# Kernel optimization log

Measured on AMD Instinct MI355X. Metric: run time of the kernel, lower is better.

## Reference

```python
import jax, jax.numpy as jnp
import numpy as np
from jax import lax

C = 256
B, H, W = 8, 64, 64


def dwconv(x, w, b, pad):
    # x: [B,C,H,W], w: [C,1,kh,kw] depthwise (groups=C), b: [C]
    y = lax.conv_general_dilated(
        x, w,
        window_strides=(1, 1),
        padding=pad,
        dimension_numbers=('NCHW', 'OIHW', 'NCHW'),
        feature_group_count=x.shape[1],
    )
    return y + b[None, :, None, None]


def setup_inputs() -> dict:
    key = jax.random.key(0)
    ks = jax.random.split(key, 16)
    s = 0.05
    inp = {
        'x': jax.random.normal(ks[0], (B, C, H, W), jnp.float32),
        'w0':   jax.random.normal(ks[1], (C, 1, 5, 5), jnp.float32) * s,
        'b0':   jax.random.normal(ks[2], (C,), jnp.float32) * s,
        'w0_1': jax.random.normal(ks[3], (C, 1, 1, 7), jnp.float32) * s,
        'b0_1': jax.random.normal(ks[4], (C,), jnp.float32) * s,
        'w0_2': jax.random.normal(ks[5], (C, 1, 7, 1), jnp.float32) * s,
        'b0_2': jax.random.normal(ks[6], (C,), jnp.float32) * s,
        'w1_1': jax.random.normal(ks[7], (C, 1, 1, 11), jnp.float32) * s,
        'b1_1': jax.random.normal(ks[8], (C,), jnp.float32) * s,
        'w1_2': jax.random.normal(ks[9], (C, 1, 11, 1), jnp.float32) * s,
        'b1_2': jax.random.normal(ks[10], (C,), jnp.float32) * s,
        'w2_1': jax.random.normal(ks[11], (C, 1, 1, 21), jnp.float32) * s,
        'b2_1': jax.random.normal(ks[12], (C,), jnp.float32) * s,
        'w2_2': jax.random.normal(ks[13], (C, 1, 21, 1), jnp.float32) * s,
        'b2_2': jax.random.normal(ks[14], (C,), jnp.float32) * s,
    }
    return inp


def reference(x, w0, b0, w0_1, b0_1, w0_2, b0_2,
              w1_1, b1_1, w1_2, b1_2, w2_1, b2_1, w2_2, b2_2):
    # 5x5 depthwise, pad 2
    attn = dwconv(x, w0, b0, ((2, 2), (2, 2)))
    # stage 0: 1x7 / 7x1 strips
    a0x = dwconv(attn, w0_1, b0_1, ((0, 0), (3, 3)))
    a0y = dwconv(attn, w0_2, b0_2, ((3, 3), (0, 0)))
    attn_0 = a0x * a0y
    # stage 1: 1x11 / 11x1 strips
    a1x = dwconv(a0x, w1_1, b1_1, ((0, 0), (5, 5)))
    a1y = dwconv(a0y, w1_2, b1_2, ((5, 5), (0, 0)))
    attn_1 = a1x * a1y
    # stage 2: 1x21 / 21x1 strips
    a2x = dwconv(a1x, w2_1, b2_1, ((0, 0), (10, 10)))
    a2y = dwconv(a1y, w2_2, b2_2, ((10, 10), (0, 0)))
    attn_2 = a2x * a2y
    return (attn_0, attn_1, attn_2)
```

## Files before the change

kernel.cpp:

```cpp
#include <hip/hip_runtime.h>


#define YS 68
#define R1_SZ 4624
#define LDS_WORDS (R1_SZ + 4352)

__device__ __forceinline__ float dpp_prev(float v) {
    return __int_as_float(__builtin_amdgcn_update_dpp(
        0, __float_as_int(v), 0x111, 0xF, 0xF, false));
}
__device__ __forceinline__ float dpp_next(float v) {
    return __int_as_float(__builtin_amdgcn_update_dpp(
        0, __float_as_int(v), 0x101, 0xF, 0xF, false));
}
__device__ __forceinline__ void ld4(const float* p, float* f) {
    float4 q = *(const float4*)p;
    f[0] = q.x; f[1] = q.y; f[2] = q.z; f[3] = q.w;
}
__device__ __forceinline__ void st4(float* p, float a, float b, float c, float d) {
    float4 q; q.x = a; q.y = b; q.z = c; q.w = d;
    *(float4*)p = q;
}

__global__ __launch_bounds__(256, 4)
void msca_fused(const float* __restrict__ x,
                const float* __restrict__ w0,   const float* __restrict__ b0,
                const float* __restrict__ w0_1, const float* __restrict__ b0_1,
                const float* __restrict__ w0_2, const float* __restrict__ b0_2,
                const float* __restrict__ w1_1, const float* __restrict__ b1_1,
                const float* __restrict__ w1_2, const float* __restrict__ b1_2,
                const float* __restrict__ w2_1, const float* __restrict__ b2_1,
                const float* __restrict__ w2_2, const float* __restrict__ b2_2,
                float* __restrict__ out)
{
    __shared__ __align__(16) float lds[LDS_WORDS];
    float* R1 = lds;
    float* R2 = lds + R1_SZ;

    const int t     = threadIdx.x;
    const int plane = blockIdx.x;
    const int ch    = plane & 255;
    const int r  = t >> 2;
    const int jg = t & 3;
    const int j0 = jg << 4;
    const int c  = t & 63;
    const int i0 = (t >> 6) << 4;

    const float* xg = x + (size_t)plane * 4096;
    float* o0 = out + (size_t)plane * 4096;
    float* o1 = o0 + 8388608;
    float* o2 = o1 + 8388608;

    float xR[16];
    #pragma unroll
    for (int k = 0; k < 4; k++) ld4(&xg[r * 64 + j0 + 4 * k], &xR[4 * k]);

    #pragma unroll
    for (int k0 = 0; k0 < 2; k0++) {
        int k = t + 256 * k0;
        if (k < 272) R1[k < 136 ? k : k + 4352] = 0.f;
    }
    if (t < 64) {
        int b = (t + 2) * YS;
        R1[b] = 0.f; R1[b + 1] = 0.f; R1[b + 66] = 0.f; R1[b + 67] = 0.f;
    }
    {
        float* row = &R1[(r + 2) * YS];
        float2 e0; e0.x = xR[0];  e0.y = xR[1];  *(float2*)&row[j0 + 2]  = e0;
        st4(&row[j0 + 4],  xR[2],  xR[3],  xR[4],  xR[5]);
        st4(&row[j0 + 8],  xR[6],  xR[7],  xR[8],  xR[9]);
        st4(&row[j0 + 12], xR[10], xR[11], xR[12], xR[13]);
        float2 e1; e1.x = xR[14]; e1.y = xR[15]; *(float2*)&row[j0 + 16] = e1;
    }
    __syncthreads();

    float attnR[16];
    {
        const float bb = b0[ch];
        #pragma unroll
        for (int j = 0; j < 16; j++) attnR[j] = bb;
        #pragma unroll
        for (int dr = 0; dr < 5; dr++) {
            float f[20];
            if (dr == 2) {
                float e0 = dpp_prev(xR[14]), e1 = dpp_prev(xR[15]);
                float e2 = dpp_next(xR[0]),  e3 = dpp_next(xR[1]);
                f[0] = jg ? e0 : 0.f;  f[1] = jg ? e1 : 0.f;
                #pragma unroll
                for (int k = 0; k < 16; k++) f[2 + k] = xR[k];
                f[18] = (jg < 3) ? e2 : 0.f;  f[19] = (jg < 3) ? e3 : 0.f;
            } else {
                const float* row = &R1[(r + dr) * YS + j0];
                #pragma unroll
                for (int k = 0; k < 5; k++) ld4(&row[4 * k], &f[4 * k]);
            }
            #pragma unroll
            for (int v = 0; v < 5; v++) {
                const float ww = w0[ch * 25 + dr * 5 + v];
                #pragma unroll
                for (int j = 0; j < 16; j++) attnR[j] += ww * f[j + v];
            }
        }
        float* row = &R2[r * YS];
        st4(&row[j0],      attnR[0],  attnR[1],  attnR[2],  attnR[3]);
        st4(&row[j0 + 4],  attnR[4],  attnR[5],  attnR[6],  attnR[7]);
        st4(&row[j0 + 8],  attnR[8],  attnR[9],  attnR[10], attnR[11]);
        st4(&row[j0 + 12], attnR[12], attnR[13], attnR[14], attnR[15]);
    }
    __syncthreads();

    float a0xR[16];
    {
        const float bb = b0_1[ch];
        float av[22];
        float p13 = dpp_prev(attnR[13]), p14 = dpp_prev(attnR[14]), p15 = dpp_prev(attnR[15]);
        float n0  = dpp_next(attnR[0]),  n1  = dpp_next(attnR[1]),  n2  = dpp_next(attnR[2]);
        av[0] = jg ? p13 : 0.f;  av[1] = jg ? p14 : 0.f;  av[2] = jg ? p15 : 0.f;
        #pragma unroll
        for (int k = 0; k < 16; k++) av[3 + k] = attnR[k];
        av[19] = (jg < 3) ? n0 : 0.f;  av[20] = (jg < 3) ? n1 : 0.f;  av[21] = (jg < 3) ? n2 : 0.f;
        #pragma unroll
        for (int j = 0; j < 16; j++) a0xR[j] = bb;
        #pragma unroll
        for (int v = 0; v < 7; v++) {
            const float ww = w0_1[ch * 7 + v];
            #pragma unroll
            for (int j = 0; j < 16; j++) a0xR[j] += ww * av[j + v];
        }
    }
    float a0yR[16];
    {
        const float bb = b0_2[ch];
        float cv[22];
        #pragma unroll
        for (int d = 0; d < 22; d++) {
            const int ir = i0 + d - 3;
            cv[d] = ((unsigned)ir <= 63u) ? R2[ir * YS + c] : 0.f;
        }
        #pragma unroll
        for (int ii = 0; ii < 16; ii++) a0yR[ii] = bb;
        #pragma unroll
        for (int u = 0; u < 7; u++) {
            const float ww = w0_2[ch * 7 + u];
            #pragma unroll
            for (int ii = 0; ii < 16; ii++) a0yR[ii] += ww * cv[ii + u];
        }
        #pragma unroll
        for (int ii = 0; ii < 16; ii++) R1[(i0 + ii) * YS + c] = a0yR[ii];
    }
    __syncthreads();

    #pragma unroll
    for (int k = 0; k < 4; k++) {
        float f[4]; ld4(&R1[r * YS + j0 + 4 * k], f);
        st4(&o0[r * 64 + j0 + 4 * k],
            a0xR[4 * k] * f[0], a0xR[4 * k + 1] * f[1],
            a0xR[4 * k + 2] * f[2], a0xR[4 * k + 3] * f[3]);
    }
    float a1xR[16];
    {
        const float bb = b1_1[ch];
        float xv[26];
        #pragma unroll
        for (int d = 0; d < 5; d++) {
            float p = dpp_prev(a0xR[11 + d]);
            float n = dpp_next(a0xR[d]);
            xv[d]      = jg ? p : 0.f;
            xv[21 + d] = (jg < 3) ? n : 0.f;
        }
        #pragma unroll
        for (int k = 0; k < 16; k++) xv[5 + k] = a0xR[k];
        #pragma unroll
        for (int j = 0; j < 16; j++) a1xR[j] = bb;
        #pragma unroll
        for (int v = 0; v < 11; v++) {
            const float ww = w1_1[ch * 11 + v];
            #pragma unroll
            for (int j = 0; j < 16; j++) a1xR[j] += ww * xv[j + v];
        }
    }
    float a1yR[16];
    {
        const float bb = b1_2[ch];
        float yv[26];
        #pragma unroll
        for (int d = 0; d < 5; d++)  yv[d]      = i0        ? R1[(i0 - 5 + d) * YS + c]  : 0.f;
        #pragma unroll
        for (int k = 0; k < 16; k++) yv[5 + k]  = a0yR[k];
        #pragma unroll
        for (int d = 0; d < 5; d++)  yv[21 + d] = (i0 < 48) ? R1[(i0 + 16 + d) * YS + c] : 0.f;
        #pragma unroll
        for (int ii = 0; ii < 16; ii++) a1yR[ii] = bb;
        #pragma unroll
        for (int u = 0; u < 11; u++) {
            const float ww = w1_2[ch * 11 + u];
            #pragma unroll
            for (int ii = 0; ii < 16; ii++) a1yR[ii] += ww * yv[ii + u];
        }
        #pragma unroll
        for (int ii = 0; ii < 16; ii++) R2[(i0 + ii) * YS + c] = a1yR[ii];
    }
    __syncthreads();

    #pragma unroll
    for (int k = 0; k < 4; k++) {
        float f[4]; ld4(&R2[r * YS + j0 + 4 * k], f);
        st4(&o1[r * 64 + j0 + 4 * k],
            a1xR[4 * k] * f[0], a1xR[4 * k + 1] * f[1],
            a1xR[4 * k + 2] * f[2], a1xR[4 * k + 3] * f[3]);
    }
    float a2xR[16];
    {
        const float bb = b2_1[ch];
        float xv[36];
        #pragma unroll
        for (int d = 0; d < 10; d++) {
            float p = dpp_prev(a1xR[6 + d]);
            float n = dpp_next(a1xR[d]);
            xv[d]      = jg ? p : 0.f;
            xv[26 + d] = (jg < 3) ? n : 0.f;
        }
        #pragma unroll
        for (int k = 0; k < 16; k++) xv[10 + k] = a1xR[k];
        #pragma unroll
        for (int j = 0; j < 16; j++) a2xR[j] = bb;
        #pragma unroll
        for (int v = 0; v < 21; v++) {
            const float ww = w2_1[ch * 21 + v];
            #pragma unroll
            for (int j = 0; j < 16; j++) a2xR[j] += ww * xv[j + v];
        }
    }
    {
        const float bb = b2_2[ch];
        float yv[36];
        #pragma unroll
        for (int d = 0; d < 10; d++) yv[d]      = i0        ? R2[(i0 - 10 + d) * YS + c] : 0.f;
        #pragma unroll
        for (int k = 0; k < 16; k++) yv[10 + k] = a1yR[k];
        #pragma unroll
        for (int d = 0; d < 10; d++) yv[26 + d] = (i0 < 48) ? R2[(i0 + 16 + d) * YS + c] : 0.f;
        float a2yR[16];
        #pragma unroll
        for (int ii = 0; ii < 16; ii++) a2yR[ii] = bb;
        #pragma unroll
        for (int u = 0; u < 21; u++) {
            const float ww = w2_2[ch * 21 + u];
            #pragma unroll
            for (int ii = 0; ii < 16; ii++) a2yR[ii] += ww * yv[ii + u];
        }
        #pragma unroll
        for (int ii = 0; ii < 16; ii++) R1[(i0 + ii) * YS + c] = a2yR[ii];
    }
    __syncthreads();

    #pragma unroll
    for (int k = 0; k < 4; k++) {
        float f[4]; ld4(&R1[r * YS + j0 + 4 * k], f);
        st4(&o2[r * 64 + j0 + 4 * k],
            a2xR[4 * k] * f[0], a2xR[4 * k + 1] * f[1],
            a2xR[4 * k + 2] * f[2], a2xR[4 * k + 3] * f[3]);
    }
}

extern "C" void kernel_launch(void* const* d_in, const int* in_sizes, int n_in,
                              void* d_out, int out_size, void* d_ws, size_t ws_size,
                              hipStream_t stream) {
    msca_fused<<<2048, 256, 0, stream>>>(
        (const float*)d_in[0],
        (const float*)d_in[1],  (const float*)d_in[2],
        (const float*)d_in[3],  (const float*)d_in[4],
        (const float*)d_in[5],  (const float*)d_in[6],
        (const float*)d_in[7],  (const float*)d_in[8],
        (const float*)d_in[9],  (const float*)d_in[10],
        (const float*)d_in[11], (const float*)d_in[12],
        (const float*)d_in[13], (const float*)d_in[14],
        (float*)d_out);
}
```

Measured before the change: 46.05 us.

## Process two channel planes per block to amortize barriers and add ILP

Each block now handles two (batch, channel) planes instead of one, with each stage looping over both planes between barriers. This halves the grid, roughly doubles LDS per block, and lowers launch bounds to 2 blocks per CU. The aim is to share each __syncthreads across two planes and give the scheduler independent work to interleave. In exchange, register pressure rises sharply (several 2x16 arrays live at once), which risks spills and lower occupancy.

```diff
diff --git a/kernel.cpp b/kernel.cpp
--- a/kernel.cpp
+++ b/kernel.cpp
@@ -2,8 +2,9 @@
 
 
 #define YS 68
-#define R1_SZ 4624
-#define LDS_WORDS (R1_SZ + 4352)
+#define R1W 4624
+#define R2W 4352
+#define LDS_WORDS (2 * (R1W + R2W))
 
 __device__ __forceinline__ float dpp_prev(float v) {
     return __int_as_float(__builtin_amdgcn_update_dpp(
@@ -22,7 +23,7 @@
     *(float4*)p = q;
 }
 
-__global__ __launch_bounds__(256, 4)
+__global__ __launch_bounds__(256, 2)
 void msca_fused(const float* __restrict__ x,
                 const float* __restrict__ w0,   const float* __restrict__ b0,
                 const float* __restrict__ w0_1, const float* __restrict__ b0_1,
@@ -34,63 +35,66 @@
                 float* __restrict__ out)
 {
     __shared__ __align__(16) float lds[LDS_WORDS];
-    float* R1 = lds;
-    float* R2 = lds + R1_SZ;
-
-    const int t     = threadIdx.x;
-    const int plane = blockIdx.x;
-    const int ch    = plane & 255;
+
+    const int t  = threadIdx.x;
     const int r  = t >> 2;
     const int jg = t & 3;
     const int j0 = jg << 4;
     const int c  = t & 63;
     const int i0 = (t >> 6) << 4;
 
-    const float* xg = x + (size_t)plane * 4096;
-    float* o0 = out + (size_t)plane * 4096;
-    float* o1 = o0 + 8388608;
-    float* o2 = o1 + 8388608;
-
-    float xR[16];
-    #pragma unroll
-    for (int k = 0; k < 4; k++) ld4(&xg[r * 64 + j0 + 4 * k], &xR[4 * k]);
-
-    #pragma unroll
-    for (int k0 = 0; k0 < 2; k0++) {
-        int k = t + 256 * k0;
-        if (k < 272) R1[k < 136 ? k : k + 4352] = 0.f;
-    }
-    if (t < 64) {
-        int b = (t + 2) * YS;
-        R1[b] = 0.f; R1[b + 1] = 0.f; R1[b + 66] = 0.f; R1[b + 67] = 0.f;
-    }
-    {
-        float* row = &R1[(r + 2) * YS];
-        float2 e0; e0.x = xR[0];  e0.y = xR[1];  *(float2*)&row[j0 + 2]  = e0;
-        st4(&row[j0 + 4],  xR[2],  xR[3],  xR[4],  xR[5]);
-        st4(&row[j0 + 8],  xR[6],  xR[7],  xR[8],  xR[9]);
-        st4(&row[j0 + 12], xR[10], xR[11], xR[12], xR[13]);
-        float2 e1; e1.x = xR[14]; e1.y = xR[15]; *(float2*)&row[j0 + 16] = e1;
-    }
-    __syncthreads();
-
-    float attnR[16];
-    {
+    const int plane0 = blockIdx.x * 2;
+
+    float xR[2][16], attnR[2][16], a0xR[2][16], a0yR[2][16];
+    float a1xR[2][16], a1yR[2][16], a2xR[2][16];
+
+    #pragma unroll
+    for (int p = 0; p < 2; p++) {
+        const float* xg = x + (size_t)(plane0 + p) * 4096;
+        #pragma unroll
+        for (int k = 0; k < 4; k++) ld4(&xg[r * 64 + j0 + 4 * k], &xR[p][4 * k]);
+    }
+    #pragma unroll
+    for (int p = 0; p < 2; p++) {
+        float* R1p = lds + p * R1W;
+        #pragma unroll
+        for (int k0 = 0; k0 < 2; k0++) {
+            int k = t + 256 * k0;
+            if (k < 272) R1p[k < 136 ? k : k + 4352] = 0.f;
+        }
+        if (t < 64) {
+            int b = (t + 2) * YS;
+            R1p[b] = 0.f; R1p[b + 1] = 0.f; R1p[b + 66] = 0.f; R1p[b + 67] = 0.f;
+        }
+        float* row = &R1p[(r + 2) * YS];
+        float2 e0; e0.x = xR[p][0];  e0.y = xR[p][1];  *(float2*)&row[j0 + 2]  = e0;
+        st4(&row[j0 + 4],  xR[p][2],  xR[p][3],  xR[p][4],  xR[p][5]);
+        st4(&row[j0 + 8],  xR[p][6],  xR[p][7],  xR[p][8],  xR[p][9]);
+        st4(&row[j0 + 12], xR[p][10], xR[p][11], xR[p][12], xR[p][13]);
+        float2 e1; e1.x = xR[p][14]; e1.y = xR[p][15]; *(float2*)&row[j0 + 16] = e1;
+    }
+    __syncthreads();
+
+    #pragma unroll
+    for (int p = 0; p < 2; p++) {
+        const int ch = (plane0 + p) & 255;
+        float* R1p = lds + p * R1W;
+        float* R2p = lds + 2 * R1W + p * R2W;
         const float bb = b0[ch];
         #pragma unroll
-        for (int j = 0; j < 16; j++) attnR[j] = bb;
+        for (int j = 0; j < 16; j++) attnR[p][j] = bb;
         #pragma unroll
         for (int dr = 0; dr < 5; dr++) {
             float f[20];
             if (dr == 2) {
-                float e0 = dpp_prev(xR[14]), e1 = dpp_prev(xR[15]);
-                float e2 = dpp_next(xR[0]),  e3 = dpp_next(xR[1]);
+                float e0 = dpp_prev(xR[p][14]), e1 = dpp_prev(xR[p][15]);
+                float e2 = dpp_next(xR[p][0]),  e3 = dpp_next(xR[p][1]);
                 f[0] = jg ? e0 : 0.f;  f[1] = jg ? e1 : 0.f;
                 #pragma unroll
-                for (int k = 0; k < 16; k++) f[2 + k] = xR[k];
+                for (int k = 0; k < 16; k++) f[2 + k] = xR[p][k];
                 f[18] = (jg < 3) ? e2 : 0.f;  f[19] = (jg < 3) ? e3 : 0.f;
             } else {
-                const float* row = &R1[(r + dr) * YS + j0];
+                const float* row = &R1p[(r + dr) * YS + j0];
                 #pragma unroll
                 for (int k = 0; k < 5; k++) ld4(&row[4 * k], &f[4 * k]);
             }
@@ -98,175 +102,203 @@
             for (int v = 0; v < 5; v++) {
                 const float ww = w0[ch * 25 + dr * 5 + v];
                 #pragma unroll
-                for (int j = 0; j < 16; j++) attnR[j] += ww * f[j + v];
+                for (int j = 0; j < 16; j++) attnR[p][j] += ww * f[j + v];
             }
         }
-        float* row = &R2[r * YS];
-        st4(&row[j0],      attnR[0],  attnR[1],  attnR[2],  attnR[3]);
-        st4(&row[j0 + 4],  attnR[4],  attnR[5],  attnR[6],  attnR[7]);
-        st4(&row[j0 + 8],  attnR[8],  attnR[9],  attnR[10], attnR[11]);
-        st4(&row[j0 + 12], attnR[12], attnR[13], attnR[14], attnR[15]);
-    }
-    __syncthreads();
-
-    float a0xR[16];
-    {
+        float* row = &R2p[r * YS];
+        st4(&row[j0],      attnR[p][0],  attnR[p][1],  attnR[p][2],  attnR[p][3]);
+        st4(&row[j0 + 4],  attnR[p][4],  attnR[p][5],  attnR[p][6],  attnR[p][7]);
+        st4(&row[j0 + 8],  attnR[p][8],  attnR[p][9],  attnR[p][10], attnR[p][11]);
+        st4(&row[j0 + 12], attnR[p][12], attnR[p][13], attnR[p][14], attnR[p][15]);
+    }
+    __syncthreads();
+
+    #pragma unroll
+    for (int p = 0; p < 2; p++) {
+        const int ch = (plane0 + p) & 255;
         const float bb = b0_1[ch];
         float av[22];
-        float p13 = dpp_prev(attnR[13]), p14 = dpp_prev(attnR[14]), p15 = dpp_prev(attnR[15]);
-        float n0  = dpp_next(attnR[0]),  n1  = dpp_next(attnR[1]),  n2  = dpp_next(attnR[2]);
+        float p13 = dpp_prev(attnR[p][13]), p14 = dpp_prev(attnR[p][14]), p15 = dpp_prev(attnR[p][15]);
+        float n0  = dpp_next(attnR[p][0]),  n1  = dpp_next(attnR[p][1]),  n2  = dpp_next(attnR[p][2]);
         av[0] = jg ? p13 : 0.f;  av[1] = jg ? p14 : 0.f;  av[2] = jg ? p15 : 0.f;
         #pragma unroll
-        for (int k = 0; k < 16; k++) av[3 + k] = attnR[k];
+        for (int k = 0; k < 16; k++) av[3 + k] = attnR[p][k];
         av[19] = (jg < 3) ? n0 : 0.f;  av[20] = (jg < 3) ? n1 : 0.f;  av[21] = (jg < 3) ? n2 : 0.f;
         #pragma unroll
-        for (int j = 0; j < 16; j++) a0xR[j] = bb;
+        for (int j = 0; j < 16; j++) a0xR[p][j] = bb;
         #pragma unroll
         for (int v = 0; v < 7; v++) {
             const float ww = w0_1[ch * 7 + v];
             #pragma unroll
-            for (int j = 0; j < 16; j++) a0xR[j] += ww * av[j + v];
-        }
-    }
-    float a0yR[16];
-    {
+            for (int j = 0; j < 16; j++) a0xR[p][j] += ww * av[j + v];
+        }
+    }
+    #pragma unroll
+    for (int p = 0; p < 2; p++) {
+        const int ch = (plane0 + p) & 255;
+        float* R1p = lds + p * R1W;
+        float* R2p = lds + 2 * R1W + p * R2W;
         const float bb = b0_2[ch];
         float cv[22];
         #pragma unroll
         for (int d = 0; d < 22; d++) {
             const int ir = i0 + d - 3;
-            cv[d] = ((unsigned)ir <= 63u) ? R2[ir * YS + c] : 0.f;
-        }
-        #pragma unroll
-        for (int ii = 0; ii < 16; ii++) a0yR[ii] = bb;
+            cv[d] = ((unsigned)ir <= 63u) ? R2p[ir * YS + c] : 0.f;
+        }
+        #pragma unroll
+        for (int ii = 0; ii < 16; ii++) a0yR[p][ii] = bb;
         #pragma unroll
         for (int u = 0; u < 7; u++) {
             const float ww = w0_2[ch * 7 + u];
             #pragma unroll
-            for (int ii = 0; ii < 16; ii++) a0yR[ii] += ww * cv[ii + u];
-        }
-        #pragma unroll
-        for (int ii = 0; ii < 16; ii++) R1[(i0 + ii) * YS + c] = a0yR[ii];
-    }
-    __syncthreads();
-
-    #pragma unroll
-    for (int k = 0; k < 4; k++) {
-        float f[4]; ld4(&R1[r * YS + j0 + 4 * k], f);
-        st4(&o0[r * 64 + j0 + 4 * k],
-            a0xR[4 * k] * f[0], a0xR[4 * k + 1] * f[1],
-            a0xR[4 * k + 2] * f[2], a0xR[4 * k + 3] * f[3]);
-    }
-    float a1xR[16];
-    {
+            for (int ii = 0; ii < 16; ii++) a0yR[p][ii] += ww * cv[ii + u];
+        }
+        #pragma unroll
+        for (int ii = 0; ii < 16; ii++) R1p[(i0 + ii) * YS + c] = a0yR[p][ii];
+    }
+    __syncthreads();
+
+    #pragma unroll
+    for (int p = 0; p < 2; p++) {
+        float* R1p = lds + p * R1W;
+        float* o0 = out + (size_t)(plane0 + p) * 4096;
+        #pragma unroll
+        for (int k = 0; k < 4; k++) {
+            float f[4]; ld4(&R1p[r * YS + j0 + 4 * k], f);
+            st4(&o0[r * 64 + j0 + 4 * k],
+                a0xR[p][4 * k] * f[0], a0xR[p][4 * k + 1] * f[1],
+                a0xR[p][4 * k + 2] * f[2], a0xR[p][4 * k + 3] * f[3]);
+        }
+    }
+    #pragma unroll
+    for (int p = 0; p < 2; p++) {
+        const int ch = (plane0 + p) & 255;
         const float bb = b1_1[ch];
         float xv[26];
         #pragma unroll
         for (int d = 0; d < 5; d++) {
-            float p = dpp_prev(a0xR[11 + d]);
-            float n = dpp_next(a0xR[d]);
-            xv[d]      = jg ? p : 0.f;
-            xv[21 + d] = (jg < 3) ? n : 0.f;
-        }
-        #pragma unroll
-        for (int k = 0; k < 16; k++) xv[5 + k] = a0xR[k];
-        #pragma unroll
-        for (int j = 0; j < 16; j++) a1xR[j] = bb;
+            float pp = dpp_prev(a0xR[p][11 + d]);
+            float nn = dpp_next(a0xR[p][d]);
+            xv[d]      = jg ? pp : 0.f;
+            xv[21 + d] = (jg < 3) ? nn : 0.f;
+        }
+        #pragma unroll
+        for (int k = 0; k < 16; k++) xv[5 + k] = a0xR[p][k];
+        #pragma unroll
+        for (int j = 0; j < 16; j++) a1xR[p][j] = bb;
         #pragma unroll
         for (int v = 0; v < 11; v++) {
             const float ww = w1_1[ch * 11 + v];
             #pragma unroll
-            for (int j = 0; j < 16; j++) a1xR[j] += ww * xv[j + v];
-        }
-    }
-    float a1yR[16];
-    {
+            for (int j = 0; j < 16; j++) a1xR[p][j] += ww * xv[j + v];
+        }
+    }
+    #pragma unroll
+    for (int p = 0; p < 2; p++) {
+        const int ch = (plane0 + p) & 255;
+        float* R1p = lds + p * R1W;
+        float* R2p = lds + 2 * R1W + p * R2W;
         const float bb = b1_2[ch];
         float yv[26];
         #pragma unroll
-        for (int d = 0; d < 5; d++)  yv[d]      = i0        ? R1[(i0 - 5 + d) * YS + c]  : 0.f;
-        #pragma unroll
-        for (int k = 0; k < 16; k++) yv[5 + k]  = a0yR[k];
-        #pragma unroll
-        for (int d = 0; d < 5; d++)  yv[21 + d] = (i0 < 48) ? R1[(i0 + 16 + d) * YS + c] : 0.f;
-        #pragma unroll
-        for (int ii = 0; ii < 16; ii++) a1yR[ii] = bb;
+        for (int d = 0; d < 5; d++)  yv[d]      = i0        ? R1p[(i0 - 5 + d) * YS + c]  : 0.f;
+        #pragma unroll
+        for (int k = 0; k < 16; k++) yv[5 + k]  = a0yR[p][k];
+        #pragma unroll
+        for (int d = 0; d < 5; d++)  yv[21 + d] = (i0 < 48) ? R1p[(i0 + 16 + d) * YS + c] : 0.f;
+        #pragma unroll
+        for (int ii = 0; ii < 16; ii++) a1yR[p][ii] = bb;
         #pragma unroll
         for (int u = 0; u < 11; u++) {
             const float ww = w1_2[ch * 11 + u];
             #pragma unroll
-            for (int ii = 0; ii < 16; ii++) a1yR[ii] += ww * yv[ii + u];
-        }
-        #pragma unroll
-        for (int ii = 0; ii < 16; ii++) R2[(i0 + ii) * YS + c] = a1yR[ii];
-    }
-    __syncthreads();
-
-    #pragma unroll
-    for (int k = 0; k < 4; k++) {
-        float f[4]; ld4(&R2[r * YS + j0 + 4 * k], f);
-        st4(&o1[r * 64 + j0 + 4 * k],
-            a1xR[4 * k] * f[0], a1xR[4 * k + 1] * f[1],
-            a1xR[4 * k + 2] * f[2], a1xR[4 * k + 3] * f[3]);
-    }
-    float a2xR[16];
-    {
+            for (int ii = 0; ii < 16; ii++) a1yR[p][ii] += ww * yv[ii + u];
+        }
+        #pragma unroll
+        for (int ii = 0; ii < 16; ii++) R2p[(i0 + ii) * YS + c] = a1yR[p][ii];
+    }
+    __syncthreads();
+
+    #pragma unroll
+    for (int p = 0; p < 2; p++) {
+        float* R2p = lds + 2 * R1W + p * R2W;
+        float* o1 = out + 8388608 + (size_t)(plane0 + p) * 4096;
+        #pragma unroll
+        for (int k = 0; k < 4; k++) {
+            float f[4]; ld4(&R2p[r * YS + j0 + 4 * k], f);
+            st4(&o1[r * 64 + j0 + 4 * k],
+                a1xR[p][4 * k] * f[0], a1xR[p][4 * k + 1] * f[1],
+                a1xR[p][4 * k + 2] * f[2], a1xR[p][4 * k + 3] * f[3]);
+        }
+    }
+    #pragma unroll
+    for (int p = 0; p < 2; p++) {
+        const int ch = (plane0 + p) & 255;
         const float bb = b2_1[ch];
         float xv[36];
         #pragma unroll
         for (int d = 0; d < 10; d++) {
-            float p = dpp_prev(a1xR[6 + d]);
-            float n = dpp_next(a1xR[d]);
-            xv[d]      = jg ? p : 0.f;
-            xv[26 + d] = (jg < 3) ? n : 0.f;
-        }
-        #pragma unroll
-        for (int k = 0; k < 16; k++) xv[10 + k] = a1xR[k];
-        #pragma unroll
-        for (int j = 0; j < 16; j++) a2xR[j] = bb;
+            float pp = dpp_prev(a1xR[p][6 + d]);
+            float nn = dpp_next(a1xR[p][d]);
+            xv[d]      = jg ? pp : 0.f;
+            xv[26 + d] = (jg < 3) ? nn : 0.f;
+        }
+        #pragma unroll
+        for (int k = 0; k < 16; k++) xv[10 + k] = a1xR[p][k];
+        #pragma unroll
+        for (int j = 0; j < 16; j++) a2xR[p][j] = bb;
         #pragma unroll
         for (int v = 0; v < 21; v++) {
             const float ww = w2_1[ch * 21 + v];
             #pragma unroll
-            for (int j = 0; j < 16; j++) a2xR[j] += ww * xv[j + v];
-        }
-    }
-    {
+            for (int j = 0; j < 16; j++) a2xR[p][j] += ww * xv[j + v];
+        }
+    }
+    #pragma unroll
+    for (int p = 0; p < 2; p++) {
+        const int ch = (plane0 + p) & 255;
+        float* R1p = lds + p * R1W;
+        float* R2p = lds + 2 * R1W + p * R2W;
         const float bb = b2_2[ch];
         float yv[36];
         #pragma unroll
-        for (int d = 0; d < 10; d++) yv[d]      = i0        ? R2[(i0 - 10 + d) * YS + c] : 0.f;
-        #pragma unroll
-        for (int k = 0; k < 16; k++) yv[10 + k] = a1yR[k];
-        #pragma unroll
-        for (int d = 0; d < 10; d++) yv[26 + d] = (i0 < 48) ? R2[(i0 + 16 + d) * YS + c] : 0.f;
-        float a2yR[16];
-        #pragma unroll
-        for (int ii = 0; ii < 16; ii++) a2yR[ii] = bb;
+        for (int d = 0; d < 10; d++) yv[d]      = i0        ? R2p[(i0 - 10 + d) * YS + c] : 0.f;
+        #pragma unroll
+        for (int k = 0; k < 16; k++) yv[10 + k] = a1yR[p][k];
+        #pragma unroll
+        for (int d = 0; d < 10; d++) yv[26 + d] = (i0 < 48) ? R2p[(i0 + 16 + d) * YS + c] : 0.f;
+        float a2y[16];
+        #pragma unroll
+        for (int ii = 0; ii < 16; ii++) a2y[ii] = bb;
         #pragma unroll
         for (int u = 0; u < 21; u++) {
             const float ww = w2_2[ch * 21 + u];
             #pragma unroll
-            for (int ii = 0; ii < 16; ii++) a2yR[ii] += ww * yv[ii + u];
-        }
-        #pragma unroll
-        for (int ii = 0; ii < 16; ii++) R1[(i0 + ii) * YS + c] = a2yR[ii];
-    }
-    __syncthreads();
-
-    #pragma unroll
-    for (int k = 0; k < 4; k++) {
-        float f[4]; ld4(&R1[r * YS + j0 + 4 * k], f);
-        st4(&o2[r * 64 + j0 + 4 * k],
-            a2xR[4 * k] * f[0], a2xR[4 * k + 1] * f[1],
-            a2xR[4 * k + 2] * f[2], a2xR[4 * k + 3] * f[3]);
+            for (int ii = 0; ii < 16; ii++) a2y[ii] += ww * yv[ii + u];
+        }
+        #pragma unroll
+        for (int ii = 0; ii < 16; ii++) R1p[(i0 + ii) * YS + c] = a2y[ii];
+    }
+    __syncthreads();
+
+    #pragma unroll
+    for (int p = 0; p < 2; p++) {
+        float* R1p = lds + p * R1W;
+        float* o2 = out + 2 * 8388608 + (size_t)(plane0 + p) * 4096;
+        #pragma unroll
+        for (int k = 0; k < 4; k++) {
+            float f[4]; ld4(&R1p[r * YS + j0 + 4 * k], f);
+            st4(&o2[r * 64 + j0 + 4 * k],
+                a2xR[p][4 * k] * f[0], a2xR[p][4 * k + 1] * f[1],
+                a2xR[p][4 * k + 2] * f[2], a2xR[p][4 * k + 3] * f[3]);
+        }
     }
 }
 
 extern "C" void kernel_launch(void* const* d_in, const int* in_sizes, int n_in,
                               void* d_out, int out_size, void* d_ws, size_t ws_size,
                               hipStream_t stream) {
-    msca_fused<<<2048, 256, 0, stream>>>(
+    msca_fused<<<1024, 256, 0, stream>>>(
         (const float*)d_in[0],
         (const float*)d_in[1],  (const float*)d_in[2],
         (const float*)d_in[3],  (const float*)d_in[4],
```

New measurement: 55.10 us. 19.6% more time.

## Vectorize depthwise conv accumulations with packed float2 FMAs and defer output stores

Applied to the files above, without the earlier changes.

Rewrites every stencil accumulation to operate on float2 pairs through a templated helper, so even-offset taps can map to packed FMA (v_pk_fma_f32) while odd taps stay scalar. Window arrays are rearranged into pair layout with padding slots. The stage-0 and stage-1 output products are computed early and their global stores are delayed until after later syncs, overlapping them with subsequent compute. This aims to cut VALU instruction count but raises register pressure under the 4-waves launch bound.

```diff
diff --git a/kernel.cpp b/kernel.cpp
--- a/kernel.cpp
+++ b/kernel.cpp
@@ -2,8 +2,11 @@
 
 
 #define YS 68
-#define R1_SZ 4624
-#define LDS_WORDS (R1_SZ + 4352)
+#define R1W 4624
+#define R2W 4352
+#define LDS_WORDS (R1W + R2W)
+
+typedef float v2f __attribute__((ext_vector_type(2)));
 
 __device__ __forceinline__ float dpp_prev(float v) {
     return __int_as_float(__builtin_amdgcn_update_dpp(
@@ -13,13 +16,34 @@
     return __int_as_float(__builtin_amdgcn_update_dpp(
         0, __float_as_int(v), 0x101, 0xF, 0xF, false));
 }
-__device__ __forceinline__ void ld4(const float* p, float* f) {
+__device__ __forceinline__ void ld4p(const float* p, v2f* w) {
     float4 q = *(const float4*)p;
-    f[0] = q.x; f[1] = q.y; f[2] = q.z; f[3] = q.w;
-}
-__device__ __forceinline__ void st4(float* p, float a, float b, float c, float d) {
-    float4 q; q.x = a; q.y = b; q.z = c; q.w = d;
+    w[0].x = q.x; w[0].y = q.y; w[1].x = q.z; w[1].y = q.w;
+}
+__device__ __forceinline__ void st4p(float* p, v2f a, v2f b) {
+    float4 q; q.x = a.x; q.y = a.y; q.z = b.x; q.w = b.y;
     *(float4*)p = q;
+}
+
+template<int K, int TAPOFF>
+__device__ __forceinline__ void conv_acc(const float* __restrict__ wrow,
+                                         const v2f* wnd, v2f* A) {
+    #pragma unroll
+    for (int v = 0; v < K; v++) {
+        const float w = wrow[v];
+        const int u = v + TAPOFF;
+        if ((u & 1) == 0) {
+            v2f wv; wv.x = w; wv.y = w;
+            #pragma unroll
+            for (int k = 0; k < 8; k++) A[k] += wv * wnd[(u >> 1) + k];
+        } else {
+            #pragma unroll
+            for (int k = 0; k < 8; k++) {
+                A[k].x += w * wnd[(u >> 1) + k].y;
+                A[k].y += w * wnd[(u >> 1) + k + 1].x;
+            }
+        }
+    }
 }
 
 __global__ __launch_bounds__(256, 4)
@@ -35,25 +59,26 @@
 {
     __shared__ __align__(16) float lds[LDS_WORDS];
     float* R1 = lds;
-    float* R2 = lds + R1_SZ;
-
-    const int t     = threadIdx.x;
-    const int plane = blockIdx.x;
-    const int ch    = plane & 255;
+    float* R2 = lds + R1W;
+
+    const int t  = threadIdx.x;
     const int r  = t >> 2;
     const int jg = t & 3;
     const int j0 = jg << 4;
     const int c  = t & 63;
     const int i0 = (t >> 6) << 4;
 
+    const int plane = blockIdx.x;
+    const int ch    = plane & 255;
+
     const float* xg = x + (size_t)plane * 4096;
     float* o0 = out + (size_t)plane * 4096;
     float* o1 = o0 + 8388608;
     float* o2 = o1 + 8388608;
 
-    float xR[16];
-    #pragma unroll
-    for (int k = 0; k < 4; k++) ld4(&xg[r * 64 + j0 + 4 * k], &xR[4 * k]);
+    v2f xR2[8];
+    #pragma unroll
+    for (int m = 0; m < 4; m++) ld4p(&xg[r * 64 + j0 + 4 * m], &xR2[2 * m]);
 
     #pragma unroll
     for (int k0 = 0; k0 < 2; k0++) {
@@ -66,200 +91,210 @@
     }
     {
         float* row = &R1[(r + 2) * YS];
-        float2 e0; e0.x = xR[0];  e0.y = xR[1];  *(float2*)&row[j0 + 2]  = e0;
-        st4(&row[j0 + 4],  xR[2],  xR[3],  xR[4],  xR[5]);
-        st4(&row[j0 + 8],  xR[6],  xR[7],  xR[8],  xR[9]);
-        st4(&row[j0 + 12], xR[10], xR[11], xR[12], xR[13]);
-        float2 e1; e1.x = xR[14]; e1.y = xR[15]; *(float2*)&row[j0 + 16] = e1;
-    }
-    __syncthreads();
-
-    float attnR[16];
+        row[j0 + 2] = xR2[0].x;  row[j0 + 3] = xR2[0].y;
+        st4p(&row[j0 + 4],  xR2[1], xR2[2]);
+        st4p(&row[j0 + 8],  xR2[3], xR2[4]);
+        st4p(&row[j0 + 12], xR2[5], xR2[6]);
+        row[j0 + 16] = xR2[7].x; row[j0 + 17] = xR2[7].y;
+    }
+    __syncthreads();
+
+    v2f attn2[8];
     {
         const float bb = b0[ch];
         #pragma unroll
-        for (int j = 0; j < 16; j++) attnR[j] = bb;
+        for (int k = 0; k < 8; k++) { attn2[k].x = bb; attn2[k].y = bb; }
         #pragma unroll
         for (int dr = 0; dr < 5; dr++) {
-            float f[20];
+            v2f wnd[10];
             if (dr == 2) {
-                float e0 = dpp_prev(xR[14]), e1 = dpp_prev(xR[15]);
-                float e2 = dpp_next(xR[0]),  e3 = dpp_next(xR[1]);
-                f[0] = jg ? e0 : 0.f;  f[1] = jg ? e1 : 0.f;
+                float e0 = dpp_prev(xR2[7].x), e1 = dpp_prev(xR2[7].y);
+                float n0 = dpp_next(xR2[0].x), n1 = dpp_next(xR2[0].y);
+                wnd[0].x = jg ? e0 : 0.f;  wnd[0].y = jg ? e1 : 0.f;
                 #pragma unroll
-                for (int k = 0; k < 16; k++) f[2 + k] = xR[k];
-                f[18] = (jg < 3) ? e2 : 0.f;  f[19] = (jg < 3) ? e3 : 0.f;
+                for (int k = 0; k < 8; k++) wnd[1 + k] = xR2[k];
+                wnd[9].x = (jg < 3) ? n0 : 0.f;  wnd[9].y = (jg < 3) ? n1 : 0.f;
             } else {
                 const float* row = &R1[(r + dr) * YS + j0];
                 #pragma unroll
-                for (int k = 0; k < 5; k++) ld4(&row[4 * k], &f[4 * k]);
+                for (int m = 0; m < 5; m++) ld4p(&row[4 * m], &wnd[2 * m]);
             }
-            #pragma unroll
-            for (int v = 0; v < 5; v++) {
-                const float ww = w0[ch * 25 + dr * 5 + v];
-                #pragma unroll
-                for (int j = 0; j < 16; j++) attnR[j] += ww * f[j + v];
-            }
+            conv_acc<5, 0>(w0 + ch * 25 + dr * 5, wnd, attn2);
         }
         float* row = &R2[r * YS];
-        st4(&row[j0],      attnR[0],  attnR[1],  attnR[2],  attnR[3]);
-        st4(&row[j0 + 4],  attnR[4],  attnR[5],  attnR[6],  attnR[7]);
-        st4(&row[j0 + 8],  attnR[8],  attnR[9],  attnR[10], attnR[11]);
-        st4(&row[j0 + 12], attnR[12], attnR[13], attnR[14], attnR[15]);
-    }
-    __syncthreads();
-
-    float a0xR[16];
+        st4p(&row[j0],      attn2[0], attn2[1]);
+        st4p(&row[j0 + 4],  attn2[2], attn2[3]);
+        st4p(&row[j0 + 8],  attn2[4], attn2[5]);
+        st4p(&row[j0 + 12], attn2[6], attn2[7]);
+    }
+    __syncthreads();
+
+    v2f a0x2[8];
     {
         const float bb = b0_1[ch];
-        float av[22];
-        float p13 = dpp_prev(attnR[13]), p14 = dpp_prev(attnR[14]), p15 = dpp_prev(attnR[15]);
-        float n0  = dpp_next(attnR[0]),  n1  = dpp_next(attnR[1]),  n2  = dpp_next(attnR[2]);
-        av[0] = jg ? p13 : 0.f;  av[1] = jg ? p14 : 0.f;  av[2] = jg ? p15 : 0.f;
-        #pragma unroll
-        for (int k = 0; k < 16; k++) av[3 + k] = attnR[k];
-        av[19] = (jg < 3) ? n0 : 0.f;  av[20] = (jg < 3) ? n1 : 0.f;  av[21] = (jg < 3) ? n2 : 0.f;
-        #pragma unroll
-        for (int j = 0; j < 16; j++) a0xR[j] = bb;
-        #pragma unroll
-        for (int v = 0; v < 7; v++) {
-            const float ww = w0_1[ch * 7 + v];
-            #pragma unroll
-            for (int j = 0; j < 16; j++) a0xR[j] += ww * av[j + v];
-        }
-    }
-    float a0yR[16];
+        #pragma unroll
+        for (int k = 0; k < 8; k++) { a0x2[k].x = bb; a0x2[k].y = bb; }
+        v2f wnd[12];
+        float p13 = dpp_prev(attn2[6].y), p14 = dpp_prev(attn2[7].x), p15 = dpp_prev(attn2[7].y);
+        float n0 = dpp_next(attn2[0].x), n1 = dpp_next(attn2[0].y), n2 = dpp_next(attn2[1].x);
+        wnd[0].x = 0.f;               wnd[0].y = jg ? p13 : 0.f;
+        wnd[1].x = jg ? p14 : 0.f;    wnd[1].y = jg ? p15 : 0.f;
+        #pragma unroll
+        for (int k = 0; k < 8; k++) wnd[2 + k] = attn2[k];
+        wnd[10].x = (jg < 3) ? n0 : 0.f;  wnd[10].y = (jg < 3) ? n1 : 0.f;
+        wnd[11].x = (jg < 3) ? n2 : 0.f;  wnd[11].y = 0.f;
+        conv_acc<7, 1>(w0_1 + ch * 7, wnd, a0x2);
+    }
+    v2f a0y2[8];
     {
         const float bb = b0_2[ch];
-        float cv[22];
-        #pragma unroll
-        for (int d = 0; d < 22; d++) {
-            const int ir = i0 + d - 3;
-            cv[d] = ((unsigned)ir <= 63u) ? R2[ir * YS + c] : 0.f;
-        }
-        #pragma unroll
-        for (int ii = 0; ii < 16; ii++) a0yR[ii] = bb;
-        #pragma unroll
-        for (int u = 0; u < 7; u++) {
-            const float ww = w0_2[ch * 7 + u];
-            #pragma unroll
-            for (int ii = 0; ii < 16; ii++) a0yR[ii] += ww * cv[ii + u];
-        }
-        #pragma unroll
-        for (int ii = 0; ii < 16; ii++) R1[(i0 + ii) * YS + c] = a0yR[ii];
-    }
-    __syncthreads();
-
-    #pragma unroll
-    for (int k = 0; k < 4; k++) {
-        float f[4]; ld4(&R1[r * YS + j0 + 4 * k], f);
-        st4(&o0[r * 64 + j0 + 4 * k],
-            a0xR[4 * k] * f[0], a0xR[4 * k + 1] * f[1],
-            a0xR[4 * k + 2] * f[2], a0xR[4 * k + 3] * f[3]);
-    }
-    float a1xR[16];
+        #pragma unroll
+        for (int k = 0; k < 8; k++) { a0y2[k].x = bb; a0y2[k].y = bb; }
+        v2f wnd[12];
+        #define GATT(ir) (((unsigned)(ir) <= 63u) ? R2[(ir) * YS + c] : 0.f)
+        wnd[0].x = 0.f;             wnd[0].y = GATT(i0 - 3);
+        wnd[1].x = GATT(i0 - 2);    wnd[1].y = GATT(i0 - 1);
+        #pragma unroll
+        for (int m = 0; m < 8; m++) {
+            wnd[2 + m].x = R2[(i0 + 2 * m) * YS + c];
+            wnd[2 + m].y = R2[(i0 + 2 * m + 1) * YS + c];
+        }
+        wnd[10].x = GATT(i0 + 16);  wnd[10].y = GATT(i0 + 17);
+        wnd[11].x = GATT(i0 + 18);  wnd[11].y = 0.f;
+        #undef GATT
+        conv_acc<7, 1>(w0_2 + ch * 7, wnd, a0y2);
+        #pragma unroll
+        for (int m = 0; m < 8; m++) {
+            R1[(i0 + 2 * m) * YS + c]     = a0y2[m].x;
+            R1[(i0 + 2 * m + 1) * YS + c] = a0y2[m].y;
+        }
+    }
+    __syncthreads();
+
+    v2f prod0[8];
+    #pragma unroll
+    for (int m = 0; m < 4; m++) {
+        v2f p[2]; ld4p(&R1[r * YS + j0 + 4 * m], p);
+        prod0[2 * m]     = a0x2[2 * m] * p[0];
+        prod0[2 * m + 1] = a0x2[2 * m + 1] * p[1];
+    }
+    v2f a1x2[8];
     {
         const float bb = b1_1[ch];
-        float xv[26];
-        #pragma unroll
-        for (int d = 0; d < 5; d++) {
-            float p = dpp_prev(a0xR[11 + d]);
-            float n = dpp_next(a0xR[d]);
-            xv[d]      = jg ? p : 0.f;
-            xv[21 + d] = (jg < 3) ? n : 0.f;
-        }
-        #pragma unroll
-        for (int k = 0; k < 16; k++) xv[5 + k] = a0xR[k];
-        #pragma unroll
-        for (int j = 0; j < 16; j++) a1xR[j] = bb;
-        #pragma unroll
-        for (int v = 0; v < 11; v++) {
-            const float ww = w1_1[ch * 11 + v];
-            #pragma unroll
-            for (int j = 0; j < 16; j++) a1xR[j] += ww * xv[j + v];
-        }
-    }
-    float a1yR[16];
+        #pragma unroll
+        for (int k = 0; k < 8; k++) { a1x2[k].x = bb; a1x2[k].y = bb; }
+        v2f wnd[14];
+        float p11 = dpp_prev(a0x2[5].y), p12 = dpp_prev(a0x2[6].x), p13 = dpp_prev(a0x2[6].y);
+        float p14 = dpp_prev(a0x2[7].x), p15 = dpp_prev(a0x2[7].y);
+        float n0 = dpp_next(a0x2[0].x), n1 = dpp_next(a0x2[0].y), n2 = dpp_next(a0x2[1].x);
+        float n3 = dpp_next(a0x2[1].y), n4 = dpp_next(a0x2[2].x);
+        wnd[0].x = 0.f;             wnd[0].y = jg ? p11 : 0.f;
+        wnd[1].x = jg ? p12 : 0.f;  wnd[1].y = jg ? p13 : 0.f;
+        wnd[2].x = jg ? p14 : 0.f;  wnd[2].y = jg ? p15 : 0.f;
+        #pragma unroll
+        for (int k = 0; k < 8; k++) wnd[3 + k] = a0x2[k];
+        wnd[11].x = (jg < 3) ? n0 : 0.f;  wnd[11].y = (jg < 3) ? n1 : 0.f;
+        wnd[12].x = (jg < 3) ? n2 : 0.f;  wnd[12].y = (jg < 3) ? n3 : 0.f;
+        wnd[13].x = (jg < 3) ? n4 : 0.f;  wnd[13].y = 0.f;
+        conv_acc<11, 1>(w1_1 + ch * 11, wnd, a1x2);
+    }
+    v2f a1y2[8];
     {
         const float bb = b1_2[ch];
-        float yv[26];
-        #pragma unroll
-        for (int d = 0; d < 5; d++)  yv[d]      = i0        ? R1[(i0 - 5 + d) * YS + c]  : 0.f;
-        #pragma unroll
-        for (int k = 0; k < 16; k++) yv[5 + k]  = a0yR[k];
-        #pragma unroll
-        for (int d = 0; d < 5; d++)  yv[21 + d] = (i0 < 48) ? R1[(i0 + 16 + d) * YS + c] : 0.f;
-        #pragma unroll
-        for (int ii = 0; ii < 16; ii++) a1yR[ii] = bb;
-        #pragma unroll
-        for (int u = 0; u < 11; u++) {
-            const float ww = w1_2[ch * 11 + u];
-            #pragma unroll
-            for (int ii = 0; ii < 16; ii++) a1yR[ii] += ww * yv[ii + u];
-        }
-        #pragma unroll
-        for (int ii = 0; ii < 16; ii++) R2[(i0 + ii) * YS + c] = a1yR[ii];
-    }
-    __syncthreads();
-
-    #pragma unroll
-    for (int k = 0; k < 4; k++) {
-        float f[4]; ld4(&R2[r * YS + j0 + 4 * k], f);
-        st4(&o1[r * 64 + j0 + 4 * k],
-            a1xR[4 * k] * f[0], a1xR[4 * k + 1] * f[1],
-            a1xR[4 * k + 2] * f[2], a1xR[4 * k + 3] * f[3]);
-    }
-    float a2xR[16];
+        #pragma unroll
+        for (int k = 0; k < 8; k++) { a1y2[k].x = bb; a1y2[k].y = bb; }
+        v2f wnd[14];
+        #define GA0Y(ir) (((unsigned)(ir) <= 63u) ? R1[(ir) * YS + c] : 0.f)
+        wnd[0].x = 0.f;             wnd[0].y = GA0Y(i0 - 5);
+        wnd[1].x = GA0Y(i0 - 4);    wnd[1].y = GA0Y(i0 - 3);
+        wnd[2].x = GA0Y(i0 - 2);    wnd[2].y = GA0Y(i0 - 1);
+        #pragma unroll
+        for (int k = 0; k < 8; k++) wnd[3 + k] = a0y2[k];
+        wnd[11].x = GA0Y(i0 + 16);  wnd[11].y = GA0Y(i0 + 17);
+        wnd[12].x = GA0Y(i0 + 18);  wnd[12].y = GA0Y(i0 + 19);
+        wnd[13].x = GA0Y(i0 + 20);  wnd[13].y = 0.f;
+        #undef GA0Y
+        conv_acc<11, 1>(w1_2 + ch * 11, wnd, a1y2);
+        #pragma unroll
+        for (int m = 0; m < 8; m++) {
+            R2[(i0 + 2 * m) * YS + c]     = a1y2[m].x;
+            R2[(i0 + 2 * m + 1) * YS + c] = a1y2[m].y;
+        }
+    }
+    __syncthreads();
+
+    st4p(&o0[r * 64 + j0],      prod0[0], prod0[1]);
+    st4p(&o0[r * 64 + j0 + 4],  prod0[2], prod0[3]);
+    st4p(&o0[r * 64 + j0 + 8],  prod0[4], prod0[5]);
+    st4p(&o0[r * 64 + j0 + 12], prod0[6], prod0[7]);
+
+    v2f prod1[8];
+    #pragma unroll
+    for (int m = 0; m < 4; m++) {
+        v2f p[2]; ld4p(&R2[r * YS + j0 + 4 * m], p);
+        prod1[2 * m]     = a1x2[2 * m] * p[0];
+        prod1[2 * m + 1] = a1x2[2 * m + 1] * p[1];
+    }
+    v2f a2x2[8];
     {
         const float bb = b2_1[ch];
-        float xv[36];
+        #pragma unroll
+        for (int k = 0; k < 8; k++) { a2x2[k].x = bb; a2x2[k].y = bb; }
+        v2f wnd[18];
+        float pv[10], nv[10];
         #pragma unroll
         for (int d = 0; d < 10; d++) {
-            float p = dpp_prev(a1xR[6 + d]);
-            float n = dpp_next(a1xR[d]);
-            xv[d]      = jg ? p : 0.f;
-            xv[26 + d] = (jg < 3) ? n : 0.f;
-        }
-        #pragma unroll
-        for (int k = 0; k < 16; k++) xv[10 + k] = a1xR[k];
-        #pragma unroll
-        for (int j = 0; j < 16; j++) a2xR[j] = bb;
-        #pragma unroll
-        for (int v = 0; v < 21; v++) {
-            const float ww = w2_1[ch * 21 + v];
-            #pragma unroll
-            for (int j = 0; j < 16; j++) a2xR[j] += ww * xv[j + v];
-        }
+            int q = 6 + d;
+            float pe = dpp_prev((q & 1) ? a1x2[q >> 1].y : a1x2[q >> 1].x);
+            float ne = dpp_next((d & 1) ? a1x2[d >> 1].y : a1x2[d >> 1].x);
+            pv[d] = jg ? pe : 0.f;
+            nv[d] = (jg < 3) ? ne : 0.f;
+        }
+        #pragma unroll
+        for (int m = 0; m < 5; m++) { wnd[m].x = pv[2 * m]; wnd[m].y = pv[2 * m + 1]; }
+        #pragma unroll
+        for (int k = 0; k < 8; k++) wnd[5 + k] = a1x2[k];
+        #pragma unroll
+        for (int m = 0; m < 5; m++) { wnd[13 + m].x = nv[2 * m]; wnd[13 + m].y = nv[2 * m + 1]; }
+        conv_acc<21, 0>(w2_1 + ch * 21, wnd, a2x2);
     }
     {
         const float bb = b2_2[ch];
-        float yv[36];
-        #pragma unroll
-        for (int d = 0; d < 10; d++) yv[d]      = i0        ? R2[(i0 - 10 + d) * YS + c] : 0.f;
-        #pragma unroll
-        for (int k = 0; k < 16; k++) yv[10 + k] = a1yR[k];
-        #pragma unroll
-        for (int d = 0; d < 10; d++) yv[26 + d] = (i0 < 48) ? R2[(i0 + 16 + d) * YS + c] : 0.f;
-        float a2yR[16];
-        #pragma unroll
-        for (int ii = 0; ii < 16; ii++) a2yR[ii] = bb;
-        #pragma unroll
-        for (int u = 0; u < 21; u++) {
-            const float ww = w2_2[ch * 21 + u];
-            #pragma unroll
-            for (int ii = 0; ii < 16; ii++) a2yR[ii] += ww * yv[ii + u];
-        }
-        #pragma unroll
-        for (int ii = 0; ii < 16; ii++) R1[(i0 + ii) * YS + c] = a2yR[ii];
-    }
-    __syncthreads();
-
-    #pragma unroll
-    for (int k = 0; k < 4; k++) {
-        float f[4]; ld4(&R1[r * YS + j0 + 4 * k], f);
-        st4(&o2[r * 64 + j0 + 4 * k],
-            a2xR[4 * k] * f[0], a2xR[4 * k + 1] * f[1],
-            a2xR[4 * k + 2] * f[2], a2xR[4 * k + 3] * f[3]);
+        v2f a2y2[8];
+        #pragma unroll
+        for (int k = 0; k < 8; k++) { a2y2[k].x = bb; a2y2[k].y = bb; }
+        v2f wnd[18];
+        #define GA1Y(ir) (((unsigned)(ir) <= 63u) ? R2[(ir) * YS + c] : 0.f)
+        #pragma unroll
+        for (int m = 0; m < 5; m++) {
+            wnd[m].x = GA1Y(i0 - 10 + 2 * m);  wnd[m].y = GA1Y(i0 - 9 + 2 * m);
+        }
+        #pragma unroll
+        for (int k = 0; k < 8; k++) wnd[5 + k] = a1y2[k];
+        #pragma unroll
+        for (int m = 0; m < 5; m++) {
+            wnd[13 + m].x = GA1Y(i0 + 16 + 2 * m);  wnd[13 + m].y = GA1Y(i0 + 17 + 2 * m);
+        }
+        #undef GA1Y
+        conv_acc<21, 0>(w2_2 + ch * 21, wnd, a2y2);
+        #pragma unroll
+        for (int m = 0; m < 8; m++) {
+            R1[(i0 + 2 * m) * YS + c]     = a2y2[m].x;
+            R1[(i0 + 2 * m + 1) * YS + c] = a2y2[m].y;
+        }
+    }
+    __syncthreads();
+
+    st4p(&o1[r * 64 + j0],      prod1[0], prod1[1]);
+    st4p(&o1[r * 64 + j0 + 4],  prod1[2], prod1[3]);
+    st4p(&o1[r * 64 + j0 + 8],  prod1[4], prod1[5]);
+    st4p(&o1[r * 64 + j0 + 12], prod1[6], prod1[7]);
+    #pragma unroll
+    for (int m = 0; m < 4; m++) {
+        v2f p[2]; ld4p(&R1[r * YS + j0 + 4 * m], p);
+        v2f q0 = a2x2[2 * m] * p[0];
+        v2f q1 = a2x2[2 * m + 1] * p[1];
+        st4p(&o2[r * 64 + j0 + 4 * m], q0, q1);
     }
 }
 
```

New measurement: 49.66 us. +7.8%, slower.
